# Performance work log

Hardware: AMD Instinct MI355X
Metric: run time of the kernel (lower is better)

Reference implementation:

```python
import jax, jax.numpy as jnp
import numpy as np

# Screen constants (from init_kwargs)
RES_X, RES_Y = 1024, 1024          # camera resolution (width, height)
PIX_X, PIX_Y = 1e-5, 1e-5          # pixel size in meters
BINNING = 1
NX, NY = RES_X // BINNING, RES_Y // BINNING  # effective resolution
LEFT, RIGHT = -RES_X * PIX_X / 2.0, RES_X * PIX_X / 2.0
BOTTOM, TOP = -RES_Y * PIX_Y / 2.0, RES_Y * PIX_Y / 2.0
HSTEP, VSTEP = PIX_X * BINNING, PIX_Y * BINNING
N_PARTICLES = 16_777_216
BEAM_SIGMA = 1e-3  # 1 mm rms beam size, fits in +/-5.12 mm screen extent


def setup_inputs() -> dict:
    key = jax.random.key(0)
    kx, ky = jax.random.split(key)
    xs = jax.random.normal(kx, (N_PARTICLES,), dtype=jnp.float32) * BEAM_SIGMA
    ys = jax.random.normal(ky, (N_PARTICLES,), dtype=jnp.float32) * BEAM_SIGMA
    misalignment = jnp.zeros((2,), dtype=jnp.float32)
    return {"xs": xs, "ys": ys, "misalignment": misalignment}


def reference(xs, ys, misalignment):
    # track(): subtract screen misalignment from transverse positions
    x = xs - misalignment[0]
    y = ys - misalignment[1]
    # reading(): 2D histogram over uniform pixel bin edges (torch.histogramdd)
    ix = jnp.floor((x - LEFT) / HSTEP).astype(jnp.int32)
    iy = jnp.floor((y - BOTTOM) / VSTEP).astype(jnp.int32)
    # points exactly on the rightmost/topmost edge belong to the last bin
    ix = jnp.where(x == RIGHT, NX - 1, ix)
    iy = jnp.where(y == TOP, NY - 1, iy)
    valid = (x >= LEFT) & (x <= RIGHT) & (y >= BOTTOM) & (y <= TOP)
    ix = jnp.clip(ix, 0, NX - 1)
    iy = jnp.clip(iy, 0, NY - 1)
    # image = flipud(hist.T): hist is (nx, ny) -> image[NY-1-iy, ix]
    flat = (NY - 1 - iy) * NX + ix
    w = valid.astype(jnp.float32)
    image = jnp.zeros((NY * NX,), dtype=jnp.float32).at[flat].add(w)
    return image.reshape(NY, NX)
```

## Files before the change

### kernel.cpp

```cpp
#include <hip/hip_runtime.h>
#include <hip/hip_bf16.h>


#define NXX 1024
#define NYY 1024
#define NROWS 1024
#define K3_THREADS 512
#define K3_CHUNK 16384
#define K3_G4 (K3_CHUNK / 4)
#define K3_CAP (K3_CHUNK + 1024)
#define HCOPIES 8
#define HSTRIDE 1025

static __device__ __forceinline__ unsigned int row_of(float y) {
    const float BOTTOM = (float)(-1024.0 * 1e-5 / 2.0);
    const float TOP    = (float)( 1024.0 * 1e-5 / 2.0);
    const float INVV   = 1.0f / 1e-5f;
    if (!((y >= BOTTOM) & (y <= TOP))) return 0xFFFFFFFFu;
    int iy = __float2int_rd((y - BOTTOM) * INVV);
    iy = min(max(iy, 0), NYY - 1);
    return (unsigned int)((NYY - 1) - iy);
}

static __device__ __forceinline__ unsigned int key_of32(float x, float y) {
    unsigned int r = row_of(y);
    if (r == 0xFFFFFFFFu) return 0xFFFFFFFFu;
    const float LEFT  = (float)(-1024.0 * 1e-5 / 2.0);
    const float RIGHT = (float)( 1024.0 * 1e-5 / 2.0);
    const float INVH  = 1.0f / 1e-5f;
    unsigned int col;
    if ((x >= LEFT) & (x <= RIGHT)) {
        int ix = __float2int_rd((x - LEFT) * INVH);
        col = (unsigned int)min(max(ix, 0), NXX - 1);
    } else {
        col = 0xFFFFu;
    }
    return (r << 16) | col;
}

__global__ __launch_bounds__(256) void k1_count(
    const float4* __restrict__ ys4, const float* __restrict__ mis,
    unsigned long long* __restrict__ counts64, int n4) {
    __shared__ unsigned int lc[2 * NROWS];
    const int t = threadIdx.x;
    #pragma unroll
    for (int j = 0; j < 8; ++j) lc[t + j * 256] = 0u;
    __syncthreads();
    const unsigned int cp = (t & 1) << 10;
    const float my = mis[1];
    for (int i = blockIdx.x * blockDim.x + t; i < n4; i += gridDim.x * blockDim.x) {
        float4 yv = ys4[i];
        unsigned int r;
        r = row_of(yv.x - my); if (r != 0xFFFFFFFFu) atomicAdd(&lc[cp + r], 1u);
        r = row_of(yv.y - my); if (r != 0xFFFFFFFFu) atomicAdd(&lc[cp + r], 1u);
        r = row_of(yv.z - my); if (r != 0xFFFFFFFFu) atomicAdd(&lc[cp + r], 1u);
        r = row_of(yv.w - my); if (r != 0xFFFFFFFFu) atomicAdd(&lc[cp + r], 1u);
    }
    __syncthreads();
    #pragma unroll
    for (int p = 0; p < 2; ++p) {
        unsigned int e = lc[4 * t + 2 * p] + lc[1024 + 4 * t + 2 * p];
        unsigned int o = lc[4 * t + 2 * p + 1] + lc[1024 + 4 * t + 2 * p + 1];
        if (e | o) atomicAdd(&counts64[2 * t + p],
                             (unsigned long long)e | ((unsigned long long)o << 32));
    }
}

__global__ __launch_bounds__(1024) void k2_prefix(
    const unsigned int* __restrict__ counts,
    unsigned int* __restrict__ offsets, unsigned long long* __restrict__ cursors64) {
    __shared__ unsigned int waveSums[16], waveBase[16];
    __shared__ unsigned int sB[NROWS];
    const int t = threadIdx.x, lane = t & 63, wid = t >> 6;
    unsigned int c = counts[t];
    unsigned int incl = c;
    #pragma unroll
    for (int d = 1; d < 64; d <<= 1) {
        unsigned int v = __shfl_up(incl, d, 64);
        if (lane >= d) incl += v;
    }
    if (lane == 63) waveSums[wid] = incl;
    __syncthreads();
    if (t == 0) {
        unsigned int s = 0;
        #pragma unroll
        for (int i = 0; i < 16; ++i) { waveBase[i] = s; s += waveSums[i]; }
    }
    __syncthreads();
    unsigned int excl = waveBase[wid] + incl - c;
    offsets[t] = excl;
    sB[t] = excl;
    __syncthreads();
    if (t < NROWS / 2) {
        cursors64[t] = (unsigned long long)sB[2 * t] |
                       ((unsigned long long)sB[2 * t + 1] << 32);
    }
}

__global__ __launch_bounds__(K3_THREADS) void k3_scatter(
    const float4* __restrict__ xs4, const float4* __restrict__ ys4,
    const float* __restrict__ mis, unsigned long long* __restrict__ cursors64,
    unsigned short* __restrict__ keys, unsigned int cap) {
    __shared__ unsigned int lCount[NROWS];
    __shared__ unsigned int lAdj[NROWS];
    __shared__ unsigned int waveSums[8], waveBase[8];
    __shared__ unsigned int totalKeys;
    __shared__ unsigned int reorder[K3_CAP];

    const int t = threadIdx.x, lane = t & 63, wid = t >> 6;
    lCount[t] = 0u; lCount[t + 512] = 0u;
    __syncthreads();
    const float mx = mis[0], my = mis[1];

    const int base4 = blockIdx.x * K3_G4;
    unsigned int mykey[32];
    unsigned short myrank[32];

    #pragma unroll
    for (int j = 0; j < 8; ++j) {
        int i = base4 + j * K3_THREADS + t;
        float4 xv = xs4[i], yv = ys4[i];
        #pragma unroll
        for (int e = 0; e < 4; ++e) {
            float xx = (e == 0 ? xv.x : e == 1 ? xv.y : e == 2 ? xv.z : xv.w) - mx;
            float yy = (e == 0 ? yv.x : e == 1 ? yv.y : e == 2 ? yv.z : yv.w) - my;
            unsigned int k = key_of32(xx, yy);
            mykey[j * 4 + e] = k;
            unsigned int rk = 0;
            if (k != 0xFFFFFFFFu) rk = atomicAdd(&lCount[k >> 16], 1u);
            myrank[j * 4 + e] = (unsigned short)rk;
        }
    }
    __syncthreads();

    unsigned int c0 = lCount[2 * t], c1 = lCount[2 * t + 1];
    unsigned int p0 = (cap != 0u) ? (c0 & 1u) : 0u;
    unsigned int p1 = (cap != 0u) ? (c1 & 1u) : 0u;
    unsigned int t0 = c0 + p0, t1 = c1 + p1;
    unsigned int tsum = t0 + t1;
    unsigned int incl = tsum;
    #pragma unroll
    for (int d = 1; d < 64; d <<= 1) {
        unsigned int v = __shfl_up(incl, d, 64);
        if (lane >= d) incl += v;
    }
    if (lane == 63) waveSums[wid] = incl;
    __syncthreads();
    if (t == 0) {
        unsigned int s = 0;
        #pragma unroll
        for (int i = 0; i < 8; ++i) { waveBase[i] = s; s += waveSums[i]; }
        totalKeys = s;
    }
    __syncthreads();
    unsigned int excl = waveBase[wid] + incl - tsum;
    lCount[2 * t] = excl;
    lCount[2 * t + 1] = excl + t0;
    if (tsum) {
        unsigned long long old = atomicAdd(&cursors64[t],
            (unsigned long long)t0 | ((unsigned long long)t1 << 32));
        unsigned int b0 = (unsigned int)old;
        unsigned int b1 = (unsigned int)(old >> 32);
        if (cap != 0u) {
            b0 += (unsigned int)(2 * t) * cap;
            b1 += (unsigned int)(2 * t + 1) * cap;
        }
        lAdj[2 * t]     = b0 - excl;
        lAdj[2 * t + 1] = b1 - (excl + t0);
    }
    if (p0) reorder[excl + c0]      = ((unsigned int)(2 * t) << 16) | 0xFFFFu;
    if (p1) reorder[excl + t0 + c1] = ((unsigned int)(2 * t + 1) << 16) | 0xFFFFu;
    __syncthreads();

    #pragma unroll
    for (int j = 0; j < 32; ++j) {
        unsigned int k = mykey[j];
        if (k != 0xFFFFFFFFu) {
            reorder[lCount[k >> 16] + myrank[j]] = k;
        }
    }
    __syncthreads();

    const unsigned int total = totalKeys;
    if (cap == 0) {
        for (unsigned int j = t; j < total; j += K3_THREADS) {
            unsigned int k = reorder[j];
            keys[lAdj[k >> 16] + j] = (unsigned short)k;
        }
    } else {
        const unsigned int pairs = total >> 1;
        for (unsigned int p = t; p < pairs; p += K3_THREADS) {
            uint2 kk = *(const uint2*)&reorder[2 * p];
            unsigned int row = kk.x >> 16;
            unsigned int g = lAdj[row] + 2 * p;
            unsigned int val = (kk.x & 0xFFFFu) | (kk.y << 16);
            if (g + 2 <= (row + 1) * cap)
                *(unsigned int*)&keys[g] = val;
        }
    }
}

__global__ __launch_bounds__(1024) void k4_hist(
    const unsigned short* __restrict__ keys,
    const unsigned int* __restrict__ cnts_or_deltas,
    const unsigned int* __restrict__ offsets,
    float* __restrict__ out, unsigned int cap) {
    __shared__ unsigned int hist[HCOPIES * HSTRIDE];
    const int b = blockIdx.x;
    const int r = (b & 1) ? (512 + (b >> 1)) : (511 - (b >> 1));
    for (int t = threadIdx.x; t < HCOPIES * HSTRIDE; t += 1024) hist[t] = 0u;
    __syncthreads();
    unsigned int start, cnt;
    if (cap == 0) { start = offsets[r]; cnt = cnts_or_deltas[r]; }
    else { start = (unsigned int)r * cap; cnt = cnts_or_deltas[r];
           if (cnt > cap) cnt = cap; }
    const unsigned int copy = (threadIdx.x & (HCOPIES - 1)) * HSTRIDE;
    unsigned int head = (8u - (start & 7u)) & 7u;
    if (head > cnt) head = cnt;
    if (threadIdx.x < head) {
        unsigned int c = min((unsigned int)keys[start + threadIdx.x], 1024u);
        atomicAdd(&hist[copy + c], 1u);
    }
    const unsigned int m = cnt - head;
    const uint4* pk = (const uint4*)(keys + start + head);
    const unsigned int octs = m >> 3;
    for (unsigned int q = threadIdx.x; q < octs; q += 1024) {
        uint4 v = pk[q];
        atomicAdd(&hist[copy + min(v.x & 0xFFFFu, 1024u)], 1u);
        atomicAdd(&hist[copy + min(v.x >> 16,     1024u)], 1u);
        atomicAdd(&hist[copy + min(v.y & 0xFFFFu, 1024u)], 1u);
        atomicAdd(&hist[copy + min(v.y >> 16,     1024u)], 1u);
        atomicAdd(&hist[copy + min(v.z & 0xFFFFu, 1024u)], 1u);
        atomicAdd(&hist[copy + min(v.z >> 16,     1024u)], 1u);
        atomicAdd(&hist[copy + min(v.w & 0xFFFFu, 1024u)], 1u);
        atomicAdd(&hist[copy + min(v.w >> 16,     1024u)], 1u);
    }
    const unsigned int tail = m & 7u;
    if (threadIdx.x < tail) {
        unsigned int c = min((unsigned int)keys[start + head + (octs << 3) + threadIdx.x], 1024u);
        atomicAdd(&hist[copy + c], 1u);
    }
    __syncthreads();
    float* dst = out + (size_t)r * NXX;
    for (int v = threadIdx.x; v < NXX; v += 1024) {
        unsigned int s = 0u;
        #pragma unroll
        for (int c2 = 0; c2 < HCOPIES; ++c2) s += hist[c2 * HSTRIDE + v];
        dst[v] = (float)s;
    }
}

__global__ __launch_bounds__(256) void fallback_hist(
    const float4* __restrict__ xs4, const float4* __restrict__ ys4,
    const float* __restrict__ mis, unsigned int* __restrict__ out, int n4) {
    const float mx = mis[0], my = mis[1];
    int i = blockIdx.x * blockDim.x + threadIdx.x;
    if (i >= n4) return;
    float4 xv = xs4[i], yv = ys4[i];
    #pragma unroll
    for (int e = 0; e < 4; ++e) {
        float xx = (e == 0 ? xv.x : e == 1 ? xv.y : e == 2 ? xv.z : xv.w) - mx;
        float yy = (e == 0 ? yv.x : e == 1 ? yv.y : e == 2 ? yv.z : yv.w) - my;
        unsigned int k = key_of32(xx, yy);
        if (k != 0xFFFFFFFFu && (k & 0xFFFFu) < NXX)
            atomicAdd(&out[(k >> 16) * NXX + (k & 0xFFFFu)], 1u);
    }
}
__global__ __launch_bounds__(256) void convert_kernel(unsigned int* __restrict__ buf, int n) {
    int i = blockIdx.x * blockDim.x + threadIdx.x;
    if (i < n) { unsigned int c = buf[i]; ((float*)buf)[i] = (float)c; }
}

extern "C" void kernel_launch(void* const* d_in, const int* in_sizes, int n_in,
                              void* d_out, int out_size, void* d_ws, size_t ws_size,
                              hipStream_t stream) {
    const float* xs  = (const float*)d_in[0];
    const float* ys  = (const float*)d_in[1];
    const float* mis = (const float*)d_in[2];

    const int n  = in_sizes[0];
    const int n4 = n / 4;

    unsigned char* ws = (unsigned char*)d_ws;
    unsigned long long* cursors64 = (unsigned long long*)(ws);
    unsigned int* cursors32       = (unsigned int*)(ws);
    unsigned int* counts          = (unsigned int*)(ws);
    unsigned long long* counts64  = (unsigned long long*)(ws);
    unsigned int* offsets         = (unsigned int*)(ws + 4096);
    unsigned long long* curs_ex   = (unsigned long long*)(ws + 8192);
    unsigned short* keys          = (unsigned short*)(ws + 65536);

    unsigned int cap = 0;
    if (ws_size > 65536) {
        size_t c = (ws_size - 65536) / (NROWS * sizeof(unsigned short));
        c &= ~(size_t)63;
        if (c >= 73728) cap = (unsigned int)((c > 131072) ? 131072 : c);
    }

    const int k3_grid = n / K3_CHUNK;

    if (cap) {
        hipMemsetAsync(ws, 0, 4096, stream);
        k3_scatter<<<k3_grid, K3_THREADS, 0, stream>>>(
            (const float4*)xs, (const float4*)ys, mis, cursors64, keys, cap);
        k4_hist<<<NROWS, 1024, 0, stream>>>(keys, cursors32, offsets,
                                            (float*)d_out, cap);
        return;
    }

    const size_t exact_need = 65536 + (size_t)n * sizeof(unsigned short);
    if (ws_size < exact_need) {
        unsigned int* out_u = (unsigned int*)d_out;
        hipMemsetAsync(d_out, 0, (size_t)out_size * sizeof(float), stream);
        fallback_hist<<<(n4 + 255) / 256, 256, 0, stream>>>(
            (const float4*)xs, (const float4*)ys, mis, out_u, n4);
        const int npix = NXX * NYY;
        convert_kernel<<<(npix + 255) / 256, 256, 0, stream>>>(out_u, npix);
        return;
    }

    hipMemsetAsync(ws, 0, 4096, stream);
    k1_count<<<512, 256, 0, stream>>>((const float4*)ys, mis, counts64, n4);
    k2_prefix<<<1, 1024, 0, stream>>>(counts, offsets, curs_ex);
    k3_scatter<<<k3_grid, K3_THREADS, 0, stream>>>(
        (const float4*)xs, (const float4*)ys, mis, curs_ex, keys, 0u);
    k4_hist<<<NROWS, 1024, 0, stream>>>(keys, counts, offsets, (float*)d_out, 0u);
}
```

Baseline: 188.2 us.

## Halve scatter chunk, split row counters by parity, and split histogram rows into halves

The scatter kernel now processes 8192 particles per block and keeps two sets of per-row counters indexed by thread parity, which cuts LDS atomic contention on hot rows. The histogram kernel launches two 512-thread blocks per row, each covering one half of the columns, so the shared histogram is smaller and more blocks run at once. The cost is that every block in a row pair reads all of that row's keys and discards the half it does not own, doubling key reads in the histogram stage. Smaller scatter chunks also mean more global cursor atomics and shorter contiguous writes per row.

```diff
diff --git a/kernel.cpp b/kernel.cpp
--- a/kernel.cpp
+++ b/kernel.cpp
@@ -6,11 +6,11 @@
 #define NYY 1024
 #define NROWS 1024
 #define K3_THREADS 512
-#define K3_CHUNK 16384
+#define K3_CHUNK 8192
 #define K3_G4 (K3_CHUNK / 4)
 #define K3_CAP (K3_CHUNK + 1024)
 #define HCOPIES 8
-#define HSTRIDE 1025
+#define HSTRIDE2 513
 
 static __device__ __forceinline__ unsigned int row_of(float y) {
     const float BOTTOM = (float)(-1024.0 * 1e-5 / 2.0);
@@ -101,23 +101,25 @@
     const float4* __restrict__ xs4, const float4* __restrict__ ys4,
     const float* __restrict__ mis, unsigned long long* __restrict__ cursors64,
     unsigned short* __restrict__ keys, unsigned int cap) {
-    __shared__ unsigned int lCount[NROWS];
+    __shared__ unsigned int lCount2[2 * NROWS];
     __shared__ unsigned int lAdj[NROWS];
     __shared__ unsigned int waveSums[8], waveBase[8];
     __shared__ unsigned int totalKeys;
     __shared__ unsigned int reorder[K3_CAP];
 
     const int t = threadIdx.x, lane = t & 63, wid = t >> 6;
-    lCount[t] = 0u; lCount[t + 512] = 0u;
+    lCount2[t] = 0u; lCount2[t + 512] = 0u;
+    lCount2[t + 1024] = 0u; lCount2[t + 1536] = 0u;
     __syncthreads();
     const float mx = mis[0], my = mis[1];
+    const unsigned int parOff = (unsigned int)(t & 1) << 10;
 
     const int base4 = blockIdx.x * K3_G4;
-    unsigned int mykey[32];
-    unsigned short myrank[32];
-
-    #pragma unroll
-    for (int j = 0; j < 8; ++j) {
+    unsigned int mykey[16];
+    unsigned short myrank[16];
+
+    #pragma unroll
+    for (int j = 0; j < 4; ++j) {
         int i = base4 + j * K3_THREADS + t;
         float4 xv = xs4[i], yv = ys4[i];
         #pragma unroll
@@ -127,13 +129,16 @@
             unsigned int k = key_of32(xx, yy);
             mykey[j * 4 + e] = k;
             unsigned int rk = 0;
-            if (k != 0xFFFFFFFFu) rk = atomicAdd(&lCount[k >> 16], 1u);
+            if (k != 0xFFFFFFFFu)
+                rk = atomicAdd(&lCount2[parOff | (k >> 16)], 1u);
             myrank[j * 4 + e] = (unsigned short)rk;
         }
     }
     __syncthreads();
 
-    unsigned int c0 = lCount[2 * t], c1 = lCount[2 * t + 1];
+    unsigned int c0a = lCount2[2 * t],     c0b = lCount2[1024 + 2 * t];
+    unsigned int c1a = lCount2[2 * t + 1], c1b = lCount2[1024 + 2 * t + 1];
+    unsigned int c0 = c0a + c0b, c1 = c1a + c1b;
     unsigned int p0 = (cap != 0u) ? (c0 & 1u) : 0u;
     unsigned int p1 = (cap != 0u) ? (c1 & 1u) : 0u;
     unsigned int t0 = c0 + p0, t1 = c1 + p1;
@@ -154,8 +159,10 @@
     }
     __syncthreads();
     unsigned int excl = waveBase[wid] + incl - tsum;
-    lCount[2 * t] = excl;
-    lCount[2 * t + 1] = excl + t0;
+    lCount2[2 * t]            = excl;
+    lCount2[1024 + 2 * t]     = excl + c0a;
+    lCount2[2 * t + 1]        = excl + t0;
+    lCount2[1024 + 2 * t + 1] = excl + t0 + c1a;
     if (tsum) {
         unsigned long long old = atomicAdd(&cursors64[t],
             (unsigned long long)t0 | ((unsigned long long)t1 << 32));
@@ -173,10 +180,10 @@
     __syncthreads();
 
     #pragma unroll
-    for (int j = 0; j < 32; ++j) {
+    for (int j = 0; j < 16; ++j) {
         unsigned int k = mykey[j];
         if (k != 0xFFFFFFFFu) {
-            reorder[lCount[k >> 16] + myrank[j]] = k;
+            reorder[lCount2[parOff | (k >> 16)] + myrank[j]] = k;
         }
     }
     __syncthreads();
@@ -200,52 +207,55 @@
     }
 }
 
-__global__ __launch_bounds__(1024) void k4_hist(
+__global__ __launch_bounds__(512) void k4_hist(
     const unsigned short* __restrict__ keys,
     const unsigned int* __restrict__ cnts_or_deltas,
     const unsigned int* __restrict__ offsets,
     float* __restrict__ out, unsigned int cap) {
-    __shared__ unsigned int hist[HCOPIES * HSTRIDE];
+    __shared__ unsigned int hist[HCOPIES * HSTRIDE2];
     const int b = blockIdx.x;
-    const int r = (b & 1) ? (512 + (b >> 1)) : (511 - (b >> 1));
-    for (int t = threadIdx.x; t < HCOPIES * HSTRIDE; t += 1024) hist[t] = 0u;
+    const int rr = b >> 1;
+    const int r = (rr & 1) ? (512 + (rr >> 1)) : (511 - (rr >> 1));
+    const unsigned int lo = (unsigned int)(b & 1) << 9;
+    for (int t = threadIdx.x; t < HCOPIES * HSTRIDE2; t += 512) hist[t] = 0u;
     __syncthreads();
     unsigned int start, cnt;
     if (cap == 0) { start = offsets[r]; cnt = cnts_or_deltas[r]; }
     else { start = (unsigned int)r * cap; cnt = cnts_or_deltas[r];
            if (cnt > cap) cnt = cap; }
-    const unsigned int copy = (threadIdx.x & (HCOPIES - 1)) * HSTRIDE;
+    const unsigned int copy = (threadIdx.x & (HCOPIES - 1)) * HSTRIDE2;
     unsigned int head = (8u - (start & 7u)) & 7u;
     if (head > cnt) head = cnt;
     if (threadIdx.x < head) {
-        unsigned int c = min((unsigned int)keys[start + threadIdx.x], 1024u);
-        atomicAdd(&hist[copy + c], 1u);
+        unsigned int d = (unsigned int)keys[start + threadIdx.x] - lo;
+        if (d < 512u) atomicAdd(&hist[copy + d], 1u);
     }
     const unsigned int m = cnt - head;
     const uint4* pk = (const uint4*)(keys + start + head);
     const unsigned int octs = m >> 3;
-    for (unsigned int q = threadIdx.x; q < octs; q += 1024) {
+    for (unsigned int q = threadIdx.x; q < octs; q += 512) {
         uint4 v = pk[q];
-        atomicAdd(&hist[copy + min(v.x & 0xFFFFu, 1024u)], 1u);
-        atomicAdd(&hist[copy + min(v.x >> 16,     1024u)], 1u);
-        atomicAdd(&hist[copy + min(v.y & 0xFFFFu, 1024u)], 1u);
-        atomicAdd(&hist[copy + min(v.y >> 16,     1024u)], 1u);
-        atomicAdd(&hist[copy + min(v.z & 0xFFFFu, 1024u)], 1u);
-        atomicAdd(&hist[copy + min(v.z >> 16,     1024u)], 1u);
-        atomicAdd(&hist[copy + min(v.w & 0xFFFFu, 1024u)], 1u);
-        atomicAdd(&hist[copy + min(v.w >> 16,     1024u)], 1u);
+        unsigned int d;
+        d = (v.x & 0xFFFFu) - lo; if (d < 512u) atomicAdd(&hist[copy + d], 1u);
+        d = (v.x >> 16)     - lo; if (d < 512u) atomicAdd(&hist[copy + d], 1u);
+        d = (v.y & 0xFFFFu) - lo; if (d < 512u) atomicAdd(&hist[copy + d], 1u);
+        d = (v.y >> 16)     - lo; if (d < 512u) atomicAdd(&hist[copy + d], 1u);
+        d = (v.z & 0xFFFFu) - lo; if (d < 512u) atomicAdd(&hist[copy + d], 1u);
+        d = (v.z >> 16)     - lo; if (d < 512u) atomicAdd(&hist[copy + d], 1u);
+        d = (v.w & 0xFFFFu) - lo; if (d < 512u) atomicAdd(&hist[copy + d], 1u);
+        d = (v.w >> 16)     - lo; if (d < 512u) atomicAdd(&hist[copy + d], 1u);
     }
     const unsigned int tail = m & 7u;
     if (threadIdx.x < tail) {
-        unsigned int c = min((unsigned int)keys[start + head + (octs << 3) + threadIdx.x], 1024u);
-        atomicAdd(&hist[copy + c], 1u);
-    }
-    __syncthreads();
-    float* dst = out + (size_t)r * NXX;
-    for (int v = threadIdx.x; v < NXX; v += 1024) {
+        unsigned int d = (unsigned int)keys[start + head + (octs << 3) + threadIdx.x] - lo;
+        if (d < 512u) atomicAdd(&hist[copy + d], 1u);
+    }
+    __syncthreads();
+    float* dst = out + (size_t)r * NXX + lo;
+    for (int v = threadIdx.x; v < 512; v += 512) {
         unsigned int s = 0u;
         #pragma unroll
-        for (int c2 = 0; c2 < HCOPIES; ++c2) s += hist[c2 * HSTRIDE + v];
+        for (int c2 = 0; c2 < HCOPIES; ++c2) s += hist[c2 * HSTRIDE2 + v];
         dst[v] = (float)s;
     }
 }
@@ -303,8 +313,8 @@
         hipMemsetAsync(ws, 0, 4096, stream);
         k3_scatter<<<k3_grid, K3_THREADS, 0, stream>>>(
             (const float4*)xs, (const float4*)ys, mis, cursors64, keys, cap);
-        k4_hist<<<NROWS, 1024, 0, stream>>>(keys, cursors32, offsets,
-                                            (float*)d_out, cap);
+        k4_hist<<<2 * NROWS, 512, 0, stream>>>(keys, cursors32, offsets,
+                                               (float*)d_out, cap);
         return;
     }
 
@@ -324,5 +334,5 @@
     k2_prefix<<<1, 1024, 0, stream>>>(counts, offsets, curs_ex);
     k3_scatter<<<k3_grid, K3_THREADS, 0, stream>>>(
         (const float4*)xs, (const float4*)ys, mis, curs_ex, keys, 0u);
-    k4_hist<<<NROWS, 1024, 0, stream>>>(keys, counts, offsets, (float*)d_out, 0u);
-}
+    k4_hist<<<2 * NROWS, 512, 0, stream>>>(keys, counts, offsets, (float*)d_out, 0u);
+}
```

Result: slower. 201.6 us (+7.1%).
